# Performance work log

Measured on AMD Instinct MI355X. Metric: run time of the kernel, lower is better.

Reference implementation:

```python
import jax, jax.numpy as jnp
import numpy as np

N_NODES = 100000


def spmm(edge_src, edge_dst, edge_val, x):
    """z[dst] += val * x[src] over all edges (COO sparse-dense matmul)."""
    gathered = edge_val[:, None] * x[edge_src]  # [E, d]
    return jax.ops.segment_sum(gathered, edge_dst, num_segments=N_NODES)


def setup_inputs() -> dict:
    key = jax.random.key(0)
    k1, k2, k3, k4, k5, k6 = jax.random.split(key, 6)
    N, E, IN, H, C = N_NODES, 1600000, 256, 128, 40
    features = jax.random.normal(k1, (N, IN), dtype=jnp.float32)
    # xavier_uniform-like init
    b1 = float(np.sqrt(6.0 / (IN + H)))
    b2 = float(np.sqrt(6.0 / (H + C)))
    W1 = jax.random.uniform(k2, (IN, H), dtype=jnp.float32, minval=-b1, maxval=b1)
    W2 = jax.random.uniform(k3, (H, C), dtype=jnp.float32, minval=-b2, maxval=b2)
    edge_src = jax.random.randint(k4, (E,), 0, N, dtype=jnp.int32)
    edge_dst = jnp.sort(jax.random.randint(k5, (E,), 0, N, dtype=jnp.int32))
    # normalized-adjacency-like positive edge weights
    edge_val = jax.random.uniform(k6, (E,), dtype=jnp.float32)
    return {"features": features, "W1": W1, "W2": W2,
            "edge_src": edge_src, "edge_dst": edge_dst, "edge_val": edge_val}


def reference(features, W1, W2, edge_src, edge_dst, edge_val):
    # Decoupled GCN: all dense NN layers first (relu between, none after last) ...
    h = jax.nn.relu(features @ W1)
    h = h @ W2  # [N, num_classes]
    # ... then nlayers (=2) rounds of graph propagation (spmm aggregation)
    h = spmm(edge_src, edge_dst, edge_val, h)
    h = spmm(edge_src, edge_dst, edge_val, h)
    return h
```

## Files before the change

### kernel.cpp

```cpp
#include <hip/hip_runtime.h>
#include <cstddef>
#include <cstdint>

#define IN_DIM 256
#define H_DIM  128
#define C_DIM  40
#define BM     128
#define BK     64
#define LDT    72
#define LDH    136
#define PAD_C  64

typedef short bf16x8 __attribute__((ext_vector_type(8)));
typedef float f32x16 __attribute__((ext_vector_type(16)));
typedef uint  u32x4  __attribute__((ext_vector_type(4)));

__device__ __forceinline__ ushort f2bf(float f) {
  uint u = __builtin_bit_cast(uint, f);
  u += 0x7fffu + ((u >> 16) & 1u);
  return (ushort)(u >> 16);
}
__device__ __forceinline__ float bf2f(uint s) {
  uint u = s << 16;
  return __builtin_bit_cast(float, u);
}
__device__ __forceinline__ uint pack2bf(float a, float b) {
#if __has_builtin(__builtin_amdgcn_cvt_pk_bf16_f32)
  typedef __bf16 bf16v2 __attribute__((ext_vector_type(2)));
  bf16v2 r = __builtin_amdgcn_cvt_pk_bf16_f32(a, b);
  return __builtin_bit_cast(uint, r);
#else
  return (uint)f2bf(a) | ((uint)f2bf(b) << 16);
#endif
}

__global__ void build_row_ptr_kernel(const int* __restrict__ dst, int E,
                                     int* __restrict__ row_ptr, int n1) {
  int n = blockIdx.x * blockDim.x + threadIdx.x;
  if (n >= n1) return;
  int lo = 0, hi = E;
  while (lo < hi) {
    int mid = (lo + hi) >> 1;
    if (dst[mid] < n) lo = mid + 1; else hi = mid;
  }
  row_ptr[n] = lo;
}

__global__ void convert_weights_kernel(const float* __restrict__ W1,
                                       const float* __restrict__ W2,
                                       ushort* __restrict__ w1t,
                                       ushort* __restrict__ w2t) {
  int tid = blockIdx.x * blockDim.x + threadIdx.x;
  if (tid < IN_DIM * H_DIM) {
    int k = tid >> 7, n = tid & 127;
    w1t[n * IN_DIM + k] = f2bf(W1[tid]);
  } else {
    int i = tid - IN_DIM * H_DIM;
    int n = i >> 7, k = i & 127;
    w2t[i] = (n < C_DIM) ? f2bf(W2[k * C_DIM + n]) : (ushort)0;
  }
}

__global__ __launch_bounds__(256, 3) void fused_dense_kernel(
    const float* __restrict__ feat, const ushort* __restrict__ w1t,
    const ushort* __restrict__ w2t, ushort* __restrict__ z0, int N) {
  __shared__ __align__(16) ushort smem[26112];

  const int t = threadIdx.x;
  const int w = t >> 6, l = t & 63;
  const int nb = blockIdx.x * BM;

  f32x16 acc[4];
#pragma unroll
  for (int tn = 0; tn < 4; ++tn)
#pragma unroll
    for (int r = 0; r < 16; ++r) acc[tn][r] = 0.f;

  const int srow = t >> 1;
  const int skh  = (t & 1) << 5;
  int grow = nb + srow; if (grow >= N) grow = N - 1;
  const float*  fp = feat + (size_t)grow * IN_DIM + skh;
  const ushort* wp = w1t + (srow << 8) + skh;

  const ushort* Abase = smem + (w * 32 + (l & 31)) * LDT + ((l >> 5) << 3);
  const ushort* Bbase = smem + 128 * LDT + (l & 31) * LDT + ((l >> 5) << 3);

  for (int kc = 0; kc < IN_DIM; kc += BK) {
    const float4* f4 = (const float4*)(fp + kc);
    uint4* adst = (uint4*)(smem + srow * LDT + skh);
#pragma unroll
    for (int i = 0; i < 4; ++i) {
      float4 v0 = f4[2 * i], v1 = f4[2 * i + 1];
      uint4 pk;
      pk.x = pack2bf(v0.x, v0.y);
      pk.y = pack2bf(v0.z, v0.w);
      pk.z = pack2bf(v1.x, v1.y);
      pk.w = pack2bf(v1.z, v1.w);
      adst[i] = pk;
    }
    const uint4* bsrc = (const uint4*)(wp + kc);
    uint4* bdst = (uint4*)(smem + 128 * LDT + srow * LDT + skh);
#pragma unroll
    for (int i = 0; i < 4; ++i) bdst[i] = bsrc[i];
    __syncthreads();

#pragma unroll
    for (int ks = 0; ks < 4; ++ks) {
      bf16x8 af = *(const bf16x8*)(Abase + ks * 16);
#pragma unroll
      for (int tn = 0; tn < 4; ++tn) {
        bf16x8 bfr = *(const bf16x8*)(Bbase + tn * 32 * LDT + ks * 16);
        acc[tn] = __builtin_amdgcn_mfma_f32_32x32x16_bf16(af, bfr, acc[tn], 0, 0, 0);
      }
    }
    __syncthreads();
  }

#pragma unroll
  for (int tn = 0; tn < 4; ++tn) {
    int col = tn * 32 + (l & 31);
#pragma unroll
    for (int r = 0; r < 16; ++r) {
      int nodeLoc = (r & 3) + 8 * (r >> 2) + 4 * (l >> 5) + 32 * w;
      float v = acc[tn][r];
      smem[nodeLoc * LDH + col] = f2bf(v > 0.f ? v : 0.f);
    }
  }
  {
    int row = t >> 2, c4 = (t & 3) << 5;
    const uint4* src = (const uint4*)(w2t + row * H_DIM + c4);
    uint4* dst = (uint4*)(smem + 128 * LDH + row * LDH + c4);
    dst[0] = src[0];
    dst[1] = src[1];
    dst[2] = src[2];
    dst[3] = src[3];
  }
  __syncthreads();

  f32x16 acc2[2];
#pragma unroll
  for (int tn = 0; tn < 2; ++tn)
#pragma unroll
    for (int r = 0; r < 16; ++r) acc2[tn][r] = 0.f;

  const ushort* Hbase  = smem + (w * 32 + (l & 31)) * LDH + ((l >> 5) << 3);
  const ushort* W2base = smem + 128 * LDH + (l & 31) * LDH + ((l >> 5) << 3);
#pragma unroll
  for (int kb = 0; kb < 8; ++kb) {
    bf16x8 af = *(const bf16x8*)(Hbase + kb * 16);
#pragma unroll
    for (int tn = 0; tn < 2; ++tn) {
      bf16x8 bfr = *(const bf16x8*)(W2base + tn * 32 * LDH + kb * 16);
      acc2[tn] = __builtin_amdgcn_mfma_f32_32x32x16_bf16(af, bfr, acc2[tn], 0, 0, 0);
    }
  }

#pragma unroll
  for (int tn = 0; tn < 2; ++tn) {
    int col = tn * 32 + (l & 31);
#pragma unroll
    for (int r = 0; r < 16; ++r) {
      int node = nb + 32 * w + (r & 3) + 8 * (r >> 2) + 4 * (l >> 5);
      if (node < N) z0[(size_t)node * PAD_C + col] = f2bf(acc2[tn][r]);
    }
  }
}

__global__ __launch_bounds__(256) void spmm_kernel(
    const int* __restrict__ row_ptr, const int* __restrict__ esrc,
    const float* __restrict__ eval, const ushort* __restrict__ x,
    ushort* __restrict__ zb, float* __restrict__ zf, int N, int out_f32) {
  int node = (blockIdx.x << 2) + (threadIdx.x >> 6);
  if (node >= N) return;
  const int lane = threadIdx.x & 63;
  const int h = lane >> 3;
  const int j = lane & 7;

  int e   = row_ptr[node];
  int end = row_ptr[node + 1];

  float acc[8];
#pragma unroll
  for (int c = 0; c < 8; ++c) acc[c] = 0.f;

  for (; e + 16 <= end; e += 16) {
    int   s0 = esrc[e + h];
    int   s1 = esrc[e + 8 + h];
    float v0 = eval[e + h];
    float v1 = eval[e + 8 + h];
    u32x4 a = *(const u32x4*)(x + (size_t)s0 * PAD_C + j * 8);
    u32x4 b = *(const u32x4*)(x + (size_t)s1 * PAD_C + j * 8);
    acc[0] = fmaf(v0, bf2f(a.x & 0xffffu), acc[0]);
    acc[1] = fmaf(v0, bf2f(a.x >> 16),     acc[1]);
    acc[2] = fmaf(v0, bf2f(a.y & 0xffffu), acc[2]);
    acc[3] = fmaf(v0, bf2f(a.y >> 16),     acc[3]);
    acc[4] = fmaf(v0, bf2f(a.z & 0xffffu), acc[4]);
    acc[5] = fmaf(v0, bf2f(a.z >> 16),     acc[5]);
    acc[6] = fmaf(v0, bf2f(a.w & 0xffffu), acc[6]);
    acc[7] = fmaf(v0, bf2f(a.w >> 16),     acc[7]);
    acc[0] = fmaf(v1, bf2f(b.x & 0xffffu), acc[0]);
    acc[1] = fmaf(v1, bf2f(b.x >> 16),     acc[1]);
    acc[2] = fmaf(v1, bf2f(b.y & 0xffffu), acc[2]);
    acc[3] = fmaf(v1, bf2f(b.y >> 16),     acc[3]);
    acc[4] = fmaf(v1, bf2f(b.z & 0xffffu), acc[4]);
    acc[5] = fmaf(v1, bf2f(b.z >> 16),     acc[5]);
    acc[6] = fmaf(v1, bf2f(b.w & 0xffffu), acc[6]);
    acc[7] = fmaf(v1, bf2f(b.w >> 16),     acc[7]);
  }
  for (; e + 8 <= end; e += 8) {
    int   s = esrc[e + h];
    float v = eval[e + h];
    u32x4 u = *(const u32x4*)(x + (size_t)s * PAD_C + j * 8);
    acc[0] = fmaf(v, bf2f(u.x & 0xffffu), acc[0]);
    acc[1] = fmaf(v, bf2f(u.x >> 16),     acc[1]);
    acc[2] = fmaf(v, bf2f(u.y & 0xffffu), acc[2]);
    acc[3] = fmaf(v, bf2f(u.y >> 16),     acc[3]);
    acc[4] = fmaf(v, bf2f(u.z & 0xffffu), acc[4]);
    acc[5] = fmaf(v, bf2f(u.z >> 16),     acc[5]);
    acc[6] = fmaf(v, bf2f(u.w & 0xffffu), acc[6]);
    acc[7] = fmaf(v, bf2f(u.w >> 16),     acc[7]);
  }
  if (e < end) {
    int ei = e + h;
    int ec = ei < end ? ei : end - 1;
    int   s  = esrc[ec];
    float v0 = eval[ec];
    float v  = ei < end ? v0 : 0.f;
    u32x4 u = *(const u32x4*)(x + (size_t)s * PAD_C + j * 8);
    acc[0] = fmaf(v, bf2f(u.x & 0xffffu), acc[0]);
    acc[1] = fmaf(v, bf2f(u.x >> 16),     acc[1]);
    acc[2] = fmaf(v, bf2f(u.y & 0xffffu), acc[2]);
    acc[3] = fmaf(v, bf2f(u.y >> 16),     acc[3]);
    acc[4] = fmaf(v, bf2f(u.z & 0xffffu), acc[4]);
    acc[5] = fmaf(v, bf2f(u.z >> 16),     acc[5]);
    acc[6] = fmaf(v, bf2f(u.w & 0xffffu), acc[6]);
    acc[7] = fmaf(v, bf2f(u.w >> 16),     acc[7]);
  }

#pragma unroll
  for (int c = 0; c < 8; ++c) acc[c] += __shfl_xor(acc[c], 8);
#pragma unroll
  for (int c = 0; c < 8; ++c) acc[c] += __shfl_xor(acc[c], 16);
#pragma unroll
  for (int c = 0; c < 8; ++c) acc[c] += __shfl_xor(acc[c], 32);

  if (out_f32) {
    if (lane < 5) {
      float4 o0 = {acc[0], acc[1], acc[2], acc[3]};
      float4 o1 = {acc[4], acc[5], acc[6], acc[7]};
      float* p = zf + (size_t)node * C_DIM + j * 8;
      *(float4*)(p + 0) = o0;
      *(float4*)(p + 4) = o1;
    }
  } else {
    if (lane < 8) {
      uint4 p;
      p.x = (uint)f2bf(acc[0]) | ((uint)f2bf(acc[1]) << 16);
      p.y = (uint)f2bf(acc[2]) | ((uint)f2bf(acc[3]) << 16);
      p.z = (uint)f2bf(acc[4]) | ((uint)f2bf(acc[5]) << 16);
      p.w = (uint)f2bf(acc[6]) | ((uint)f2bf(acc[7]) << 16);
      *(uint4*)(zb + (size_t)node * PAD_C + j * 8) = p;
    }
  }
}

extern "C" void kernel_launch(void* const* d_in, const int* in_sizes, int n_in,
                              void* d_out, int out_size, void* d_ws, size_t ws_size,
                              hipStream_t stream) {
  const float* feat  = (const float*)d_in[0];
  const float* W1    = (const float*)d_in[1];
  const float* W2    = (const float*)d_in[2];
  const int*   esrc  = (const int*)d_in[3];
  const int*   edst  = (const int*)d_in[4];
  const float* evalp = (const float*)d_in[5];
  float* out = (float*)d_out;

  const int N = in_sizes[0] / IN_DIM;
  const int E = in_sizes[3];

  char* ws = (char*)d_ws;
  ushort* z0  = (ushort*)ws;
  ushort* z1  = (ushort*)(ws + (size_t)N * PAD_C * 2);
  ushort* w1t = (ushort*)(ws + (size_t)N * PAD_C * 4);
  ushort* w2t = w1t + IN_DIM * H_DIM;
  int* row_ptr = (int*)((char*)(w2t + PAD_C * H_DIM));

  build_row_ptr_kernel<<<(N + 256) / 256, 256, 0, stream>>>(edst, E, row_ptr, N + 1);
  convert_weights_kernel<<<(IN_DIM * H_DIM + PAD_C * H_DIM) / 256, 256, 0, stream>>>(
      W1, W2, w1t, w2t);
  fused_dense_kernel<<<(N + BM - 1) / BM, 256, 0, stream>>>(feat, w1t, w2t, z0, N);
  spmm_kernel<<<(N + 3) / 4, 256, 0, stream>>>(row_ptr, esrc, evalp, z0, z1, nullptr, N, 0);
  spmm_kernel<<<(N + 3) / 4, 256, 0, stream>>>(row_ptr, esrc, evalp, z1, nullptr, out, N, 1);
}
```

Baseline: 273.8 us.

## Merge setup kernels, read W2 from global, restructure SpMM edge loop

Fuses the row-pointer binary search and the weight conversion into one setup kernel, which saves a launch. The dense kernel no longer stages W2 in shared memory. It reads W2 fragments directly from global/L2, shrinking LDS so four blocks per CU fit, and drops one barrier. The SpMM kernel peels the first 32 edges into two predicated 16-edge chunks with clamped indices, followed by an 8-edge tail loop. This targets the typical degree of about 16, and the bf16 pack now uses the hardware conversion. Reading W2 from global adds latency to the second GEMM, and the peeled loads do wasted work on nodes with low degree.

```diff
diff --git a/kernel.cpp b/kernel.cpp
--- a/kernel.cpp
+++ b/kernel.cpp
@@ -34,37 +34,35 @@
 #endif
 }
 
-__global__ void build_row_ptr_kernel(const int* __restrict__ dst, int E,
-                                     int* __restrict__ row_ptr, int n1) {
-  int n = blockIdx.x * blockDim.x + threadIdx.x;
-  if (n >= n1) return;
-  int lo = 0, hi = E;
-  while (lo < hi) {
-    int mid = (lo + hi) >> 1;
-    if (dst[mid] < n) lo = mid + 1; else hi = mid;
-  }
-  row_ptr[n] = lo;
-}
-
-__global__ void convert_weights_kernel(const float* __restrict__ W1,
-                                       const float* __restrict__ W2,
-                                       ushort* __restrict__ w1t,
-                                       ushort* __restrict__ w2t) {
+__global__ void setup_kernel(const int* __restrict__ dst, int E,
+                             int* __restrict__ row_ptr, int n1,
+                             const float* __restrict__ W1,
+                             const float* __restrict__ W2,
+                             ushort* __restrict__ w1t,
+                             ushort* __restrict__ w2t) {
   int tid = blockIdx.x * blockDim.x + threadIdx.x;
-  if (tid < IN_DIM * H_DIM) {
-    int k = tid >> 7, n = tid & 127;
-    w1t[n * IN_DIM + k] = f2bf(W1[tid]);
-  } else {
-    int i = tid - IN_DIM * H_DIM;
+  if (tid < n1) {
+    int n = tid, lo = 0, hi = E;
+    while (lo < hi) {
+      int mid = (lo + hi) >> 1;
+      if (dst[mid] < n) lo = mid + 1; else hi = mid;
+    }
+    row_ptr[n] = lo;
+  } else if (tid < n1 + IN_DIM * H_DIM) {
+    int i = tid - n1;
+    int k = i >> 7, n = i & 127;
+    w1t[n * IN_DIM + k] = f2bf(W1[i]);
+  } else if (tid < n1 + IN_DIM * H_DIM + PAD_C * H_DIM) {
+    int i = tid - n1 - IN_DIM * H_DIM;
     int n = i >> 7, k = i & 127;
     w2t[i] = (n < C_DIM) ? f2bf(W2[k * C_DIM + n]) : (ushort)0;
   }
 }
 
-__global__ __launch_bounds__(256, 3) void fused_dense_kernel(
+__global__ __launch_bounds__(256, 4) void fused_dense_kernel(
     const float* __restrict__ feat, const ushort* __restrict__ w1t,
     const ushort* __restrict__ w2t, ushort* __restrict__ z0, int N) {
-  __shared__ __align__(16) ushort smem[26112];
+  __shared__ __align__(16) ushort smem[18432];
 
   const int t = threadIdx.x;
   const int w = t >> 6, l = t & 63;
@@ -126,16 +124,6 @@
       smem[nodeLoc * LDH + col] = f2bf(v > 0.f ? v : 0.f);
     }
   }
-  {
-    int row = t >> 2, c4 = (t & 3) << 5;
-    const uint4* src = (const uint4*)(w2t + row * H_DIM + c4);
-    uint4* dst = (uint4*)(smem + 128 * LDH + row * LDH + c4);
-    dst[0] = src[0];
-    dst[1] = src[1];
-    dst[2] = src[2];
-    dst[3] = src[3];
-  }
-  __syncthreads();
 
   f32x16 acc2[2];
 #pragma unroll
@@ -144,13 +132,13 @@
     for (int r = 0; r < 16; ++r) acc2[tn][r] = 0.f;
 
   const ushort* Hbase  = smem + (w * 32 + (l & 31)) * LDH + ((l >> 5) << 3);
-  const ushort* W2base = smem + 128 * LDH + (l & 31) * LDH + ((l >> 5) << 3);
+  const ushort* W2gbl  = w2t + (size_t)(l & 31) * H_DIM + ((l >> 5) << 3);
 #pragma unroll
   for (int kb = 0; kb < 8; ++kb) {
     bf16x8 af = *(const bf16x8*)(Hbase + kb * 16);
 #pragma unroll
     for (int tn = 0; tn < 2; ++tn) {
-      bf16x8 bfr = *(const bf16x8*)(W2base + tn * 32 * LDH + kb * 16);
+      bf16x8 bfr = *(const bf16x8*)(W2gbl + tn * 32 * H_DIM + kb * 16);
       acc2[tn] = __builtin_amdgcn_mfma_f32_32x32x16_bf16(af, bfr, acc2[tn], 0, 0, 0);
     }
   }
@@ -176,65 +164,88 @@
   const int h = lane >> 3;
   const int j = lane & 7;
 
-  int e   = row_ptr[node];
-  int end = row_ptr[node + 1];
+  const int e   = row_ptr[node];
+  const int end = row_ptr[node + 1];
+  const int deg = end - e;
 
   float acc[8];
 #pragma unroll
   for (int c = 0; c < 8; ++c) acc[c] = 0.f;
 
-  for (; e + 16 <= end; e += 16) {
-    int   s0 = esrc[e + h];
-    int   s1 = esrc[e + 8 + h];
-    float v0 = eval[e + h];
-    float v1 = eval[e + 8 + h];
-    u32x4 a = *(const u32x4*)(x + (size_t)s0 * PAD_C + j * 8);
-    u32x4 b = *(const u32x4*)(x + (size_t)s1 * PAD_C + j * 8);
-    acc[0] = fmaf(v0, bf2f(a.x & 0xffffu), acc[0]);
-    acc[1] = fmaf(v0, bf2f(a.x >> 16),     acc[1]);
-    acc[2] = fmaf(v0, bf2f(a.y & 0xffffu), acc[2]);
-    acc[3] = fmaf(v0, bf2f(a.y >> 16),     acc[3]);
-    acc[4] = fmaf(v0, bf2f(a.z & 0xffffu), acc[4]);
-    acc[5] = fmaf(v0, bf2f(a.z >> 16),     acc[5]);
-    acc[6] = fmaf(v0, bf2f(a.w & 0xffffu), acc[6]);
-    acc[7] = fmaf(v0, bf2f(a.w >> 16),     acc[7]);
-    acc[0] = fmaf(v1, bf2f(b.x & 0xffffu), acc[0]);
-    acc[1] = fmaf(v1, bf2f(b.x >> 16),     acc[1]);
-    acc[2] = fmaf(v1, bf2f(b.y & 0xffffu), acc[2]);
-    acc[3] = fmaf(v1, bf2f(b.y >> 16),     acc[3]);
-    acc[4] = fmaf(v1, bf2f(b.z & 0xffffu), acc[4]);
-    acc[5] = fmaf(v1, bf2f(b.z >> 16),     acc[5]);
-    acc[6] = fmaf(v1, bf2f(b.w & 0xffffu), acc[6]);
-    acc[7] = fmaf(v1, bf2f(b.w >> 16),     acc[7]);
-  }
-  for (; e + 8 <= end; e += 8) {
-    int   s = esrc[e + h];
-    float v = eval[e + h];
-    u32x4 u = *(const u32x4*)(x + (size_t)s * PAD_C + j * 8);
-    acc[0] = fmaf(v, bf2f(u.x & 0xffffu), acc[0]);
-    acc[1] = fmaf(v, bf2f(u.x >> 16),     acc[1]);
-    acc[2] = fmaf(v, bf2f(u.y & 0xffffu), acc[2]);
-    acc[3] = fmaf(v, bf2f(u.y >> 16),     acc[3]);
-    acc[4] = fmaf(v, bf2f(u.z & 0xffffu), acc[4]);
-    acc[5] = fmaf(v, bf2f(u.z >> 16),     acc[5]);
-    acc[6] = fmaf(v, bf2f(u.w & 0xffffu), acc[6]);
-    acc[7] = fmaf(v, bf2f(u.w >> 16),     acc[7]);
-  }
-  if (e < end) {
-    int ei = e + h;
-    int ec = ei < end ? ei : end - 1;
-    int   s  = esrc[ec];
-    float v0 = eval[ec];
-    float v  = ei < end ? v0 : 0.f;
-    u32x4 u = *(const u32x4*)(x + (size_t)s * PAD_C + j * 8);
-    acc[0] = fmaf(v, bf2f(u.x & 0xffffu), acc[0]);
-    acc[1] = fmaf(v, bf2f(u.x >> 16),     acc[1]);
-    acc[2] = fmaf(v, bf2f(u.y & 0xffffu), acc[2]);
-    acc[3] = fmaf(v, bf2f(u.y >> 16),     acc[3]);
-    acc[4] = fmaf(v, bf2f(u.z & 0xffffu), acc[4]);
-    acc[5] = fmaf(v, bf2f(u.z >> 16),     acc[5]);
-    acc[6] = fmaf(v, bf2f(u.w & 0xffffu), acc[6]);
-    acc[7] = fmaf(v, bf2f(u.w >> 16),     acc[7]);
+  const ushort* xj = x + j * 8;
+
+  if (deg > 0) {
+    {
+      int sl0 = h, sl1 = 8 + h;
+      int i0 = e + (sl0 < deg ? sl0 : deg - 1);
+      int i1 = e + (sl1 < deg ? sl1 : deg - 1);
+      int   s0 = esrc[i0];
+      int   s1 = esrc[i1];
+      float v0 = sl0 < deg ? eval[i0] : 0.f;
+      float v1 = sl1 < deg ? eval[i1] : 0.f;
+      u32x4 a = *(const u32x4*)(xj + (size_t)s0 * PAD_C);
+      u32x4 b = *(const u32x4*)(xj + (size_t)s1 * PAD_C);
+      acc[0] = fmaf(v0, bf2f(a.x & 0xffffu), acc[0]);
+      acc[1] = fmaf(v0, bf2f(a.x >> 16),     acc[1]);
+      acc[2] = fmaf(v0, bf2f(a.y & 0xffffu), acc[2]);
+      acc[3] = fmaf(v0, bf2f(a.y >> 16),     acc[3]);
+      acc[4] = fmaf(v0, bf2f(a.z & 0xffffu), acc[4]);
+      acc[5] = fmaf(v0, bf2f(a.z >> 16),     acc[5]);
+      acc[6] = fmaf(v0, bf2f(a.w & 0xffffu), acc[6]);
+      acc[7] = fmaf(v0, bf2f(a.w >> 16),     acc[7]);
+      acc[0] = fmaf(v1, bf2f(b.x & 0xffffu), acc[0]);
+      acc[1] = fmaf(v1, bf2f(b.x >> 16),     acc[1]);
+      acc[2] = fmaf(v1, bf2f(b.y & 0xffffu), acc[2]);
+      acc[3] = fmaf(v1, bf2f(b.y >> 16),     acc[3]);
+      acc[4] = fmaf(v1, bf2f(b.z & 0xffffu), acc[4]);
+      acc[5] = fmaf(v1, bf2f(b.z >> 16),     acc[5]);
+      acc[6] = fmaf(v1, bf2f(b.w & 0xffffu), acc[6]);
+      acc[7] = fmaf(v1, bf2f(b.w >> 16),     acc[7]);
+    }
+    if (deg > 16) {
+      {
+        int sl0 = 16 + h, sl1 = 24 + h;
+        int i0 = e + (sl0 < deg ? sl0 : deg - 1);
+        int i1 = e + (sl1 < deg ? sl1 : deg - 1);
+        int   s0 = esrc[i0];
+        int   s1 = esrc[i1];
+        float v0 = sl0 < deg ? eval[i0] : 0.f;
+        float v1 = sl1 < deg ? eval[i1] : 0.f;
+        u32x4 a = *(const u32x4*)(xj + (size_t)s0 * PAD_C);
+        u32x4 b = *(const u32x4*)(xj + (size_t)s1 * PAD_C);
+        acc[0] = fmaf(v0, bf2f(a.x & 0xffffu), acc[0]);
+        acc[1] = fmaf(v0, bf2f(a.x >> 16),     acc[1]);
+        acc[2] = fmaf(v0, bf2f(a.y & 0xffffu), acc[2]);
+        acc[3] = fmaf(v0, bf2f(a.y >> 16),     acc[3]);
+        acc[4] = fmaf(v0, bf2f(a.z & 0xffffu), acc[4]);
+        acc[5] = fmaf(v0, bf2f(a.z >> 16),     acc[5]);
+        acc[6] = fmaf(v0, bf2f(a.w & 0xffffu), acc[6]);
+        acc[7] = fmaf(v0, bf2f(a.w >> 16),     acc[7]);
+        acc[0] = fmaf(v1, bf2f(b.x & 0xffffu), acc[0]);
+        acc[1] = fmaf(v1, bf2f(b.x >> 16),     acc[1]);
+        acc[2] = fmaf(v1, bf2f(b.y & 0xffffu), acc[2]);
+        acc[3] = fmaf(v1, bf2f(b.y >> 16),     acc[3]);
+        acc[4] = fmaf(v1, bf2f(b.z & 0xffffu), acc[4]);
+        acc[5] = fmaf(v1, bf2f(b.z >> 16),     acc[5]);
+        acc[6] = fmaf(v1, bf2f(b.w & 0xffffu), acc[6]);
+        acc[7] = fmaf(v1, bf2f(b.w >> 16),     acc[7]);
+      }
+      for (int b0 = e + 32; b0 < end; b0 += 8) {
+        int sl = b0 + h;
+        int ec = sl < end ? sl : end - 1;
+        int   s = esrc[ec];
+        float v = sl < end ? eval[ec] : 0.f;
+        u32x4 u = *(const u32x4*)(xj + (size_t)s * PAD_C);
+        acc[0] = fmaf(v, bf2f(u.x & 0xffffu), acc[0]);
+        acc[1] = fmaf(v, bf2f(u.x >> 16),     acc[1]);
+        acc[2] = fmaf(v, bf2f(u.y & 0xffffu), acc[2]);
+        acc[3] = fmaf(v, bf2f(u.y >> 16),     acc[3]);
+        acc[4] = fmaf(v, bf2f(u.z & 0xffffu), acc[4]);
+        acc[5] = fmaf(v, bf2f(u.z >> 16),     acc[5]);
+        acc[6] = fmaf(v, bf2f(u.w & 0xffffu), acc[6]);
+        acc[7] = fmaf(v, bf2f(u.w >> 16),     acc[7]);
+      }
+    }
   }
 
 #pragma unroll
@@ -255,10 +266,10 @@
   } else {
     if (lane < 8) {
       uint4 p;
-      p.x = (uint)f2bf(acc[0]) | ((uint)f2bf(acc[1]) << 16);
-      p.y = (uint)f2bf(acc[2]) | ((uint)f2bf(acc[3]) << 16);
-      p.z = (uint)f2bf(acc[4]) | ((uint)f2bf(acc[5]) << 16);
-      p.w = (uint)f2bf(acc[6]) | ((uint)f2bf(acc[7]) << 16);
+      p.x = pack2bf(acc[0], acc[1]);
+      p.y = pack2bf(acc[2], acc[3]);
+      p.z = pack2bf(acc[4], acc[5]);
+      p.w = pack2bf(acc[6], acc[7]);
       *(uint4*)(zb + (size_t)node * PAD_C + j * 8) = p;
     }
   }
@@ -285,9 +296,9 @@
   ushort* w2t = w1t + IN_DIM * H_DIM;
   int* row_ptr = (int*)((char*)(w2t + PAD_C * H_DIM));
 
-  build_row_ptr_kernel<<<(N + 256) / 256, 256, 0, stream>>>(edst, E, row_ptr, N + 1);
-  convert_weights_kernel<<<(IN_DIM * H_DIM + PAD_C * H_DIM) / 256, 256, 0, stream>>>(
-      W1, W2, w1t, w2t);
+  const int setup_total = (N + 1) + IN_DIM * H_DIM + PAD_C * H_DIM;
+  setup_kernel<<<(setup_total + 255) / 256, 256, 0, stream>>>(
+      edst, E, row_ptr, N + 1, W1, W2, w1t, w2t);
   fused_dense_kernel<<<(N + BM - 1) / BM, 256, 0, stream>>>(feat, w1t, w2t, z0, N);
   spmm_kernel<<<(N + 3) / 4, 256, 0, stream>>>(row_ptr, esrc, evalp, z0, z1, nullptr, N, 0);
   spmm_kernel<<<(N + 3) / 4, 256, 0, stream>>>(row_ptr, esrc, evalp, z1, nullptr, out, N, 1);
```

Result: no change. 277.9 us (+1.5%).
